# Performance work log

Hardware: AMD Instinct MI355X
Metric: run time of the kernel (lower is better)

## Reference

```python
import jax, jax.numpy as jnp
import numpy as np

FEAT_DIM = 128
GUIDE_DIM = 128
HIDDEN = [1024, 512, 256, 128]
OUT_DIM = 2


def make_coord(shape):
    # grid-center coords in (-1, 1), matching the torch make_coord
    seqs = [(-1.0 + 1.0 / n) + (2.0 / n) * jnp.arange(n, dtype=jnp.float32) for n in shape]
    yy, xx = jnp.meshgrid(seqs[0], seqs[1], indexing='ij')
    return jnp.stack([yy, xx], axis=-1)  # [h, w, 2]


def grid_sample_nearest(img, coord):
    # img: [B, C, H, W]; coord: [B, N, 2] with coord[...,0] along H, coord[...,1] along W
    # replicates F.grid_sample(img, coord.flip(-1)..., mode='nearest', align_corners=False,
    # padding_mode='zeros') followed by permute -> [B, N, C]
    B, C, H, W = img.shape
    iy = jnp.round(((coord[..., 0] + 1.0) * H - 1.0) * 0.5)
    ix = jnp.round(((coord[..., 1] + 1.0) * W - 1.0) * 0.5)
    valid = (iy >= 0) & (iy < H) & (ix >= 0) & (ix < W)
    iyc = jnp.clip(iy, 0, H - 1).astype(jnp.int32)
    ixc = jnp.clip(ix, 0, W - 1).astype(jnp.int32)
    g = jax.vmap(lambda im, y, x: im[:, y, x])(img, iyc, ixc)  # [B, C, N]
    g = g * valid[:, None, :].astype(img.dtype)  # zero padding outside
    return jnp.transpose(g, (0, 2, 1))  # [B, N, C]


def mlp(x, params):
    for W, b in params[:-1]:
        x = jax.nn.relu(x @ W + b)
    W, b = params[-1]
    return x @ W + b


def setup_inputs() -> dict:
    key = jax.random.key(0)
    ks = jax.random.split(key, 16)
    B, h, w = 4, 64, 64
    H_hr = W_hr = 256
    N = H_hr * W_hr  # 65536 query points
    feat = jax.random.normal(ks[0], (B, FEAT_DIM, h, w), jnp.float32)
    coord = jax.random.uniform(ks[1], (B, N, 2), jnp.float32, minval=-1.0, maxval=1.0)
    hr_guide = jax.random.normal(ks[2], (B, GUIDE_DIM, H_hr, W_hr), jnp.float32)
    lr_guide = jax.random.normal(ks[3], (B, GUIDE_DIM, h, w), jnp.float32)
    in_dim = FEAT_DIM + 2 * GUIDE_DIM + 2  # 386
    dims = [in_dim] + HIDDEN + [OUT_DIM]
    inp = {"feat": feat, "coord": coord, "hr_guide": hr_guide, "lr_guide": lr_guide}
    for i in range(len(dims) - 1):
        scale = 1.0 / np.sqrt(dims[i]).astype(np.float32)
        inp[f"W{i}"] = jax.random.normal(ks[4 + 2 * i], (dims[i], dims[i + 1]), jnp.float32) * scale
        inp[f"b{i}"] = jnp.zeros((dims[i + 1],), jnp.float32)
    return inp


def reference(feat, coord, hr_guide, lr_guide, W0, b0, W1, b1, W2, b2, W3, b3, W4, b4):
    params = [(W0, b0), (W1, b1), (W2, b2), (W3, b3), (W4, b4)]
    B, C, h, w = feat.shape
    N = coord.shape[1]
    fc = make_coord((h, w))  # [h, w, 2]
    feat_coord = jnp.broadcast_to(jnp.transpose(fc, (2, 0, 1))[None], (B, 2, h, w))
    q_guide_hr = grid_sample_nearest(hr_guide, coord)  # [B, N, G]
    rx = 1.0 / h
    ry = 1.0 / w
    hw = jnp.array([h, w], dtype=coord.dtype)
    preds = []
    for vx in (-1.0, 1.0):
        for vy in (-1.0, 1.0):
            shift = jnp.array([vx * rx, vy * ry], dtype=coord.dtype)
            coord_ = coord + shift
            q_feat = grid_sample_nearest(feat, coord_)        # [B, N, C]
            q_coord = grid_sample_nearest(feat_coord, coord_)  # [B, N, 2]
            rel_coord = (coord - q_coord) * hw                 # [B, N, 2]
            q_guide_lr = grid_sample_nearest(lr_guide, coord_)  # [B, N, G]
            inp = jnp.concatenate([q_feat, q_guide_hr, q_guide_hr - q_guide_lr, rel_coord], axis=-1)
            pred = mlp(inp.reshape(B * N, -1), params).reshape(B, N, OUT_DIM)
            preds.append(pred)
    preds = jnp.stack(preds, axis=-1)  # [B, N, 2, 4]
    weight = jax.nn.softmax(preds[:, :, 1, :], axis=-1)  # [B, N, 4]
    ret = jnp.sum(preds[:, :, 0, :] * weight, axis=-1, keepdims=True)  # [B, N, 1]
    return ret
```

## Files before the change

kernel.cpp:

```cpp
#include <hip/hip_runtime.h>
#include <cstdint>
#include <cstddef>


typedef unsigned short u16;
typedef unsigned int u32;
typedef _Float16 half8 __attribute__((ext_vector_type(8)));
typedef float floatx4 __attribute__((ext_vector_type(4)));
typedef float floatx2 __attribute__((ext_vector_type(2)));
typedef u32 u32x2 __attribute__((ext_vector_type(2)));
typedef u32 u32x4 __attribute__((ext_vector_type(4)));

__device__ __forceinline__ u16 f2h(float x) {
    _Float16 h = (_Float16)x;
    return __builtin_bit_cast(unsigned short, h);
}
__device__ __forceinline__ float h2f(u16 u) {
    return (float)__builtin_bit_cast(_Float16, u);
}

__device__ __forceinline__ void cp_async16(const void* gsrc, void* lds) {
#if defined(__has_builtin) && __has_builtin(__builtin_amdgcn_global_load_lds)
    __builtin_amdgcn_global_load_lds(
        (__attribute__((address_space(1))) void*)(uintptr_t)gsrc,
        (__attribute__((address_space(3))) void*)(uint32_t)(uintptr_t)lds,
        16, 0, 0);
#else
    *(u32x4*)lds = *(const u32x4*)gsrc;
#endif
}

__global__ void transpose_chw_hwc(const float* __restrict__ src,
                                  u16* __restrict__ dst, int HW) {
    __shared__ float t[32][33];
    const int b = blockIdx.z;
    const int hw0 = blockIdx.x * 32, c0 = blockIdx.y * 32;
    const float* s = src + (size_t)b * 128 * HW;
    u16* d = dst + (size_t)b * HW * 128;
    const int tx = threadIdx.x, ty = threadIdx.y;
#pragma unroll
    for (int j = 0; j < 4; ++j)
        t[ty + j * 8][tx] = s[(size_t)(c0 + ty + j * 8) * HW + hw0 + tx];
    __syncthreads();
#pragma unroll
    for (int j = 0; j < 4; ++j)
        d[(size_t)(hw0 + ty + j * 8) * 128 + c0 + tx] = f2h(t[tx][ty + j * 8]);
}

__global__ void prep_wt(const float* __restrict__ W, u16* __restrict__ Wt,
                        int K, int N, int perm) {
    int idx = blockIdx.x * 256 + threadIdx.x;
    if (idx >= N * K) return;
    int nn = idx / K, kk = idx - nn * K;
    int ka = kk;
    if (perm) {
        int s = kk & 63;
        ka = (kk & ~63) + ((s & 3) << 4) + (s >> 2);
    }
    Wt[idx] = f2h(W[(size_t)ka * N + nn]);
}

__global__ void prep_w0(const float* __restrict__ W0, u16* __restrict__ Wt0m,
                        u16* __restrict__ Wthr) {
    int idx = blockIdx.x * 256 + threadIdx.x;
    if (idx < 1024 * 256) {
        int n = idx >> 8, k = idx & 255;
        float v = (k < 128) ? W0[(size_t)k * 1024 + n]
                            : -W0[(size_t)(128 + k) * 1024 + n];
        Wt0m[idx] = f2h(v);
    }
    if (idx < 1024 * 128) {
        int n = idx >> 7, k = idx & 127;
        Wthr[idx] = f2h(W0[(size_t)(128 + k) * 1024 + n] +
                        W0[(size_t)(256 + k) * 1024 + n]);
    }
}

__global__ __launch_bounds__(256) void gather_build(
    const float* __restrict__ coord, const u16* __restrict__ hrT,
    const u16* __restrict__ featT, const u16* __restrict__ lrT,
    u16* __restrict__ X, u16* __restrict__ Qhr, float* __restrict__ rel,
    int p0) {
    const int wid = threadIdx.x >> 6, lane = threadIdx.x & 63;
    const int pl = blockIdx.x * 4 + wid;
    const int p = p0 + pl;
    const int b = p >> 16;
    const float cy = coord[(size_t)p * 2];
    const float cx = coord[(size_t)p * 2 + 1];
    const u32* hr32 = (const u32*)hrT;
    const u32* ft32 = (const u32*)featT;
    const u32* lr32 = (const u32*)lrT;

    float fy = rintf(((cy + 1.0f) * 256.0f - 1.0f) * 0.5f);
    float fx = rintf(((cx + 1.0f) * 256.0f - 1.0f) * 0.5f);
    bool vh = (fy >= 0.0f) && (fy < 256.0f) && (fx >= 0.0f) && (fx < 256.0f);
    int iy = (int)fminf(fmaxf(fy, 0.0f), 255.0f);
    int ix = (int)fminf(fmaxf(fx, 0.0f), 255.0f);
    u32 hrv = hr32[((((size_t)b * 256 + iy) * 256 + ix) * 128 >> 1) + lane];
    if (!vh) hrv = 0u;
    ((u32*)Qhr)[(size_t)pl * 64 + lane] = hrv;

    const size_t rowbase = (size_t)pl * 4;
#pragma unroll
    for (int s = 0; s < 4; ++s) {
        float sy = (s & 2) ? 0.015625f : -0.015625f;
        float sx = (s & 1) ? 0.015625f : -0.015625f;
        float gy = rintf(((cy + sy + 1.0f) * 64.0f - 1.0f) * 0.5f);
        float gx = rintf(((cx + sx + 1.0f) * 64.0f - 1.0f) * 0.5f);
        bool v = (gy >= 0.0f) && (gy < 64.0f) && (gx >= 0.0f) && (gx < 64.0f);
        int jy = (int)fminf(fmaxf(gy, 0.0f), 63.0f);
        int jx = (int)fminf(fmaxf(gx, 0.0f), 63.0f);
        size_t g32 = ((((size_t)b * 64 + jy) * 64 + jx) * 128 >> 1) + lane;
        u32 fv = ft32[g32];
        u32 lv = lr32[g32];
        if (!v) { fv = 0u; lv = 0u; }

        u32* xr = (u32*)(X + (rowbase + s) * 256);
        xr[lane] = fv;
        xr[64 + lane] = lv;

        if (lane == 0) {
            float qcy = v ? (-0.984375f + 0.03125f * (float)jy) : 0.0f;
            float qcx = v ? (-0.984375f + 0.03125f * (float)jx) : 0.0f;
            rel[(rowbase + s) * 2 + 0] = (cy - qcy) * 64.0f;
            rel[(rowbase + s) * 2 + 1] = (cx - qcx) * 64.0f;
        }
    }
}

__global__ __launch_bounds__(512, 2) void gemm_f16_256(
    const u16* __restrict__ A, const u16* __restrict__ Bt,
    const float* __restrict__ bias, u16* __restrict__ C, int K, int N,
    int lognb, const float* __restrict__ rel, const float* __restrict__ w0tail) {
    __shared__ __align__(16) u16 sA[2][2][8192];
    __shared__ __align__(16) u16 sB[2][2][8192];
    const int tid = threadIdx.x;
    const int lane = tid & 63;
    const int wid = tid >> 6;
    const int r = lane & 15, q = lane >> 4;
    const int wm = wid >> 2, wn = wid & 3;

    const int g = blockIdx.x;
    const int n_idx = (g >> 3) & ((1 << lognb) - 1);
    const int m_idx = (g & 7) + ((g >> (3 + lognb)) << 3);
    const int n0 = n_idx << 8;
    const u32 m0 = (u32)m_idx << 8;

    const u32 srow = (u32)(tid >> 2);
    const u32 gchunk = (u32)((tid & 3) ^ ((tid >> 3) & 3));
    const u32 gaoff = (m0 + srow) * (u32)K + (gchunk << 3);
    const u32 gboff = ((u32)n0 + srow) * (u32)K + (gchunk << 3);

    auto stageA = [&](int kt, int ks, int buf) {
        const u16* gp = A + gaoff + (u32)((kt << 6) + (ks << 5));
        u16* lp = &sA[buf][ks][tid << 3];
        cp_async16(gp, lp);
        cp_async16(gp + ((u32)K << 7), lp + 4096);
    };
    auto stageB = [&](int kt, int ks, int buf) {
        const u16* gp = Bt + gboff + (u32)((kt << 6) + (ks << 5));
        u16* lp = &sB[buf][ks][tid << 3];
        cp_async16(gp, lp);
        cp_async16(gp + ((u32)K << 7), lp + 4096);
    };

    const int fs = (q ^ ((r >> 1) & 3)) << 3;
    const int abase = ((wm << 7) + r) * 32 + fs;
    const int bbase = ((wn << 6) + r) * 32 + fs;

    floatx4 acc[8][4];
#pragma unroll
    for (int mi = 0; mi < 8; ++mi)
#pragma unroll
        for (int ni = 0; ni < 4; ++ni)
            acc[mi][ni] = (floatx4){0.0f, 0.0f, 0.0f, 0.0f};

    const int nk = K >> 6;
    stageA(0, 0, 0);
    stageA(0, 1, 0);
    stageB(0, 0, 0);
    stageB(0, 1, 0);
    const int k1 = (nk > 1) ? 1 : 0;
    stageA(k1, 0, 1);
    stageA(k1, 1, 1);
    stageB(k1, 1, 1);
    asm volatile("s_waitcnt vmcnt(6)");
    __builtin_amdgcn_s_barrier();

    half8 a0[8], a1[8], bf[2], bg[2];
    for (int kt = 0; kt < nk; ++kt) {
        const int cur = kt & 1, nxt = cur ^ 1;
        const bool p1 = (kt + 1) < nk;
        const bool p2 = (kt + 2) < nk;
#pragma unroll
        for (int mi = 0; mi < 8; ++mi)
            a0[mi] = *(const half8*)&sA[cur][0][abase + (mi << 9)];
#pragma unroll
        for (int ni = 0; ni < 2; ++ni)
            bf[ni] = *(const half8*)&sB[cur][0][bbase + (ni << 9)];
        if (p1) stageB(kt + 1, 0, nxt);
#pragma unroll
        for (int mi = 0; mi < 8; ++mi)
            a1[mi] = *(const half8*)&sA[cur][1][abase + (mi << 9)];
#pragma unroll
        for (int ni = 0; ni < 2; ++ni)
            bg[ni] = *(const half8*)&sB[cur][1][bbase + (ni << 9)];
        __builtin_amdgcn_s_setprio(1);
#pragma unroll
        for (int mi = 0; mi < 8; ++mi)
#pragma unroll
            for (int ni = 0; ni < 2; ++ni)
                acc[mi][ni] = __builtin_amdgcn_mfma_f32_16x16x32_f16(
                    a0[mi], bf[ni], acc[mi][ni], 0, 0, 0);
        __builtin_amdgcn_s_setprio(0);
        __builtin_amdgcn_s_barrier();
        if (p2) stageA(kt + 2, 0, cur);
#pragma unroll
        for (int ni = 0; ni < 2; ++ni)
            bf[ni] = *(const half8*)&sB[cur][1][bbase + 1024 + (ni << 9)];
        __builtin_amdgcn_s_setprio(1);
#pragma unroll
        for (int mi = 0; mi < 8; ++mi)
#pragma unroll
            for (int ni = 0; ni < 2; ++ni)
                acc[mi][ni] = __builtin_amdgcn_mfma_f32_16x16x32_f16(
                    a1[mi], bg[ni], acc[mi][ni], 0, 0, 0);
        __builtin_amdgcn_s_setprio(0);
        __builtin_amdgcn_s_barrier();
        if (p2) stageA(kt + 2, 1, cur);
#pragma unroll
        for (int ni = 0; ni < 2; ++ni)
            bg[ni] = *(const half8*)&sB[cur][0][bbase + 1024 + (ni << 9)];
        __builtin_amdgcn_s_setprio(1);
#pragma unroll
        for (int mi = 0; mi < 8; ++mi)
#pragma unroll
            for (int ni = 0; ni < 2; ++ni)
                acc[mi][2 + ni] = __builtin_amdgcn_mfma_f32_16x16x32_f16(
                    a1[mi], bf[ni], acc[mi][2 + ni], 0, 0, 0);
        __builtin_amdgcn_s_setprio(0);
        __builtin_amdgcn_s_barrier();
        if (p2) stageB(kt + 2, 1, cur);
        __builtin_amdgcn_s_setprio(1);
#pragma unroll
        for (int mi = 0; mi < 8; ++mi)
#pragma unroll
            for (int ni = 0; ni < 2; ++ni)
                acc[mi][2 + ni] = __builtin_amdgcn_mfma_f32_16x16x32_f16(
                    a0[mi], bg[ni], acc[mi][2 + ni], 0, 0, 0);
        __builtin_amdgcn_s_setprio(0);
        if (p2) {
            asm volatile("s_waitcnt vmcnt(6)");
        } else {
            asm volatile("s_waitcnt vmcnt(0)");
        }
        __builtin_amdgcn_s_barrier();
    }

    float bias_v[4], w0a[4], w0b[4];
#pragma unroll
    for (int nig = 0; nig < 4; ++nig) {
        int col = n0 + (wn << 6) + nig * 16 + r;
        bias_v[nig] = bias[col];
        w0a[nig] = rel ? w0tail[col] : 0.0f;
        w0b[nig] = rel ? w0tail[N + col] : 0.0f;
    }
#pragma unroll
    for (int mi = 0; mi < 8; ++mi) {
#pragma unroll
        for (int rr = 0; rr < 4; ++rr) {
            u32 row = m0 + (u32)(wm << 7) + (u32)(mi << 4) + (u32)(q << 2) +
                      (u32)rr;
            float rl0 = 0.0f, rl1 = 0.0f;
            if (rel) {
                floatx2 rl = *(const floatx2*)&rel[(size_t)row * 2];
                rl0 = rl[0];
                rl1 = rl[1];
            }
            u32 pk[2];
#pragma unroll
            for (int h = 0; h < 2; ++h) {
                u32 w = 0;
#pragma unroll
                for (int j = 0; j < 2; ++j) {
                    int nig = h * 2 + j;
                    float v = acc[mi][nig][rr] + bias_v[nig];
                    if (rel) v += rl0 * w0a[nig] + rl1 * w0b[nig];
                    v = fmaxf(v, 0.0f);
                    w |= (u32)f2h(v) << (16 * j);
                }
                pk[h] = w;
            }
            *(u32x2*)(C + row * (u32)N + (u32)(n0 + (wn << 6) + (r << 2))) =
                (u32x2){pk[0], pk[1]};
        }
    }
}

__global__ __launch_bounds__(256, 3) void gemm_f16(
    const u16* __restrict__ A, const u16* __restrict__ Bt,
    const float* __restrict__ bias, u16* __restrict__ C, int K, int N,
    int lognb, const float* __restrict__ rel, const float* __restrict__ w0tail,
    const u16* __restrict__ hq, int doRelu) {
    __shared__ __align__(16) u16 As[2][128 * 64];
    __shared__ __align__(16) u16 Bs[128 * 64];
    const int tid = threadIdx.x;
    const int lane = tid & 63;
    const int wid = tid >> 6;
    const int r = lane & 15, q = lane >> 4;
    const int wm = (wid & 1) << 6, wn = (wid >> 1) << 6;

    const int g = blockIdx.x;
    const int n_idx = (g >> 3) & ((1 << lognb) - 1);
    const int m_idx = (g & 7) + ((g >> (3 + lognb)) << 3);
    const int n0 = n_idx << 7;
    const u32 m0 = (u32)m_idx << 7;

    const int srow = tid >> 3;
    const int schunk = (tid & 7) ^ (srow & 7);
    const u32 gaoff = (m0 + (u32)srow) * (u32)K + ((u32)schunk << 3);
    const u32 gboff = (u32)(n0 + srow) * (u32)K + ((u32)schunk << 3);

    auto stageA = [&](int kt, int buf) {
        const u16* gak = A + gaoff + (kt << 6);
        u16* la = &As[buf][tid * 8];
#pragma unroll
        for (int i = 0; i < 4; ++i)
            cp_async16(gak + (u32)(i << 5) * (u32)K, la + (i << 11));
    };

    u32x4 breg[4];
    auto loadB = [&](int kt) {
        const u16* gbk = Bt + gboff + (kt << 6);
#pragma unroll
        for (int i = 0; i < 4; ++i)
            breg[i] = *(const u32x4*)(gbk + (u32)(i << 5) * (u32)K);
    };
    auto writeB = [&]() {
        u16* lb = &Bs[tid * 8];
#pragma unroll
        for (int i = 0; i < 4; ++i)
            *(u32x4*)(lb + (i << 11)) = breg[i];
    };

    const int cx = (q ^ (r & 7)) << 3;
    const int arow = (wm + r) << 6, brow = (wn + r) << 6;

    floatx4 acc[4][4];
#pragma unroll
    for (int mi = 0; mi < 4; ++mi)
#pragma unroll
        for (int ni = 0; ni < 4; ++ni)
            acc[mi][ni] = (floatx4){0.0f, 0.0f, 0.0f, 0.0f};

    const int nk = K >> 6;
    loadB(0);
    stageA(0, 0);
    writeB();
    __syncthreads();

    for (int kt = 0; kt < nk; ++kt) {
        const int cur = kt & 1;
        const bool pf = (kt + 1 < nk);
        if (pf) {
            loadB(kt + 1);
            stageA(kt + 1, cur ^ 1);
        }
#pragma unroll
        for (int ks = 0; ks < 2; ++ks) {
            half8 af[4], bfr[4];
#pragma unroll
            for (int mi = 0; mi < 4; ++mi)
                af[mi] = *(const half8*)&As[cur][arow + (mi << 10) + (cx ^ (ks << 5))];
#pragma unroll
            for (int ni = 0; ni < 4; ++ni)
                bfr[ni] = *(const half8*)&Bs[brow + (ni << 10) + (cx ^ (ks << 5))];
#pragma unroll
            for (int mi = 0; mi < 4; ++mi)
#pragma unroll
                for (int ni = 0; ni < 4; ++ni)
                    acc[mi][ni] = __builtin_amdgcn_mfma_f32_16x16x32_f16(
                        af[mi], bfr[ni], acc[mi][ni], 0, 0, 0);
        }
        if (pf) {
            __syncthreads();
            writeB();
            __syncthreads();
        }
    }

    float bias_v[4], w0a[4], w0b[4];
#pragma unroll
    for (int ni = 0; ni < 4; ++ni) {
        int col = n0 + wn + ni * 16 + r;
        bias_v[ni] = bias ? bias[col] : 0.0f;
        w0a[ni] = rel ? w0tail[col] : 0.0f;
        w0b[ni] = rel ? w0tail[N + col] : 0.0f;
    }
#pragma unroll
    for (int mi = 0; mi < 4; ++mi) {
        float addv[4];
        if (hq) {
            u32 pidx = ((m0 + (u32)wm + (u32)(mi << 4)) >> 2) + (u32)q;
            u32x2 hv = *(const u32x2*)(hq + (size_t)pidx * (u32)N +
                                       (u32)(n0 + wn + (r << 2)));
            addv[0] = h2f((u16)(hv[0] & 0xffffu));
            addv[1] = h2f((u16)(hv[0] >> 16));
            addv[2] = h2f((u16)(hv[1] & 0xffffu));
            addv[3] = h2f((u16)(hv[1] >> 16));
        } else {
#pragma unroll
            for (int ni = 0; ni < 4; ++ni) addv[ni] = bias_v[ni];
        }
#pragma unroll
        for (int rr = 0; rr < 4; ++rr) {
            u32 row = m0 + wm + mi * 16 + q * 4 + rr;
            float rl0 = 0.0f, rl1 = 0.0f;
            if (rel) {
                floatx2 rl = *(const floatx2*)&rel[(size_t)row * 2];
                rl0 = rl[0];
                rl1 = rl[1];
            }
            u32 pk[2];
#pragma unroll
            for (int h = 0; h < 2; ++h) {
                u32 w = 0;
#pragma unroll
                for (int j = 0; j < 2; ++j) {
                    int ni = h * 2 + j;
                    float v = acc[mi][ni][rr] + addv[ni];
                    if (rel) v += rl0 * w0a[ni] + rl1 * w0b[ni];
                    if (doRelu) v = fmaxf(v, 0.0f);
                    w |= (u32)f2h(v) << (16 * j);
                }
                pk[h] = w;
            }
            *(u32x2*)(C + row * (u32)N + (u32)(n0 + wn + (r << 2))) =
                (u32x2){pk[0], pk[1]};
        }
    }
}

__global__ __launch_bounds__(256, 3) void gemm_l3l4(
    const u16* __restrict__ A, const u16* __restrict__ Bt,
    const float* __restrict__ b3, const float* __restrict__ W4,
    const float* __restrict__ b4, float* __restrict__ out, int p0) {
    __shared__ __align__(16) u16 As[2][128 * 64];
    __shared__ __align__(16) u16 Bs[128 * 64];
    __shared__ float sums[2][2][64][2];
    const int K = 256;
    const int tid = threadIdx.x;
    const int lane = tid & 63;
    const int wid = tid >> 6;
    const int r = lane & 15, q = lane >> 4;
    const int wm1 = wid & 1, wn1 = wid >> 1;
    const int wm = wm1 << 6, wn = wn1 << 6;
    const u32 m0 = (u32)blockIdx.x << 7;

    const int srow = tid >> 3;
    const int schunk = (tid & 7) ^ (srow & 7);
    const u32 gaoff = (m0 + (u32)srow) * (u32)K + ((u32)schunk << 3);
    const u32 gboff = (u32)srow * (u32)K + ((u32)schunk << 3);

    auto stageA = [&](int kt, int buf) {
        const u16* gak = A + gaoff + (kt << 6);
        u16* la = &As[buf][tid * 8];
#pragma unroll
        for (int i = 0; i < 4; ++i)
            cp_async16(gak + (u32)(i << 5) * (u32)K, la + (i << 11));
    };

    u32x4 breg[4];
    auto loadB = [&](int kt) {
        const u16* gbk = Bt + gboff + (kt << 6);
#pragma unroll
        for (int i = 0; i < 4; ++i)
            breg[i] = *(const u32x4*)(gbk + (u32)(i << 5) * (u32)K);
    };
    auto writeB = [&]() {
        u16* lb = &Bs[tid * 8];
#pragma unroll
        for (int i = 0; i < 4; ++i)
            *(u32x4*)(lb + (i << 11)) = breg[i];
    };

    const int cx = (q ^ (r & 7)) << 3;
    const int arow = (wm + r) << 6, brow = (wn + r) << 6;

    floatx4 acc[4][4];
#pragma unroll
    for (int mi = 0; mi < 4; ++mi)
#pragma unroll
        for (int ni = 0; ni < 4; ++ni)
            acc[mi][ni] = (floatx4){0.0f, 0.0f, 0.0f, 0.0f};

    const int nk = K >> 6;
    loadB(0);
    stageA(0, 0);
    writeB();
    __syncthreads();
    for (int kt = 0; kt < nk; ++kt) {
        const int cur = kt & 1;
        const bool pf = (kt + 1 < nk);
        if (pf) {
            loadB(kt + 1);
            stageA(kt + 1, cur ^ 1);
        }
#pragma unroll
        for (int ks = 0; ks < 2; ++ks) {
            half8 af[4], bfr[4];
#pragma unroll
            for (int mi = 0; mi < 4; ++mi)
                af[mi] = *(const half8*)&As[cur][arow + (mi << 10) + (cx ^ (ks << 5))];
#pragma unroll
            for (int ni = 0; ni < 4; ++ni)
                bfr[ni] = *(const half8*)&Bs[brow + (ni << 10) + (cx ^ (ks << 5))];
#pragma unroll
            for (int mi = 0; mi < 4; ++mi)
#pragma unroll
                for (int ni = 0; ni < 4; ++ni)
                    acc[mi][ni] = __builtin_amdgcn_mfma_f32_16x16x32_f16(
                        af[mi], bfr[ni], acc[mi][ni], 0, 0, 0);
        }
        if (pf) {
            __syncthreads();
            writeB();
            __syncthreads();
        }
    }

    float b3v[4], w40[4], w41[4];
#pragma unroll
    for (int ni = 0; ni < 4; ++ni) {
        int ch = wn + ni * 16 + r;
        b3v[ni] = b3[ch];
        w40[ni] = W4[ch * 2];
        w41[ni] = W4[ch * 2 + 1];
    }
#pragma unroll
    for (int mi = 0; mi < 4; ++mi) {
#pragma unroll
        for (int rr = 0; rr < 4; ++rr) {
            float d0 = 0.0f, d1 = 0.0f;
#pragma unroll
            for (int ni = 0; ni < 4; ++ni) {
                float v = fmaxf(acc[mi][ni][rr] + b3v[ni], 0.0f);
                d0 += v * w40[ni];
                d1 += v * w41[ni];
            }
#pragma unroll
            for (int m = 1; m <= 8; m <<= 1) {
                d0 += __shfl_xor(d0, m, 64);
                d1 += __shfl_xor(d1, m, 64);
            }
            if (r == 0) {
                int rl = mi * 16 + q * 4 + rr;
                sums[wm1][wn1][rl][0] = d0;
                sums[wm1][wn1][rl][1] = d1;
            }
        }
    }
    __syncthreads();
    if (tid < 32) {
        const int pl = tid;
        const int w = pl >> 4;
        const int rb = (pl & 15) * 4;
        float P0[4], P1[4];
#pragma unroll
        for (int s = 0; s < 4; ++s) {
            P0[s] = sums[w][0][rb + s][0] + sums[w][1][rb + s][0] + b4[0];
            P1[s] = sums[w][0][rb + s][1] + sums[w][1][rb + s][1] + b4[1];
        }
        float mx = fmaxf(fmaxf(P1[0], P1[1]), fmaxf(P1[2], P1[3]));
        float e0 = __expf(P1[0] - mx), e1 = __expf(P1[1] - mx);
        float e2 = __expf(P1[2] - mx), e3 = __expf(P1[3] - mx);
        float se = e0 + e1 + e2 + e3;
        out[p0 + (int)(m0 >> 2) + pl] =
            (P0[0] * e0 + P0[1] * e1 + P0[2] * e2 + P0[3] * e3) / se;
    }
}

extern "C" void kernel_launch(void* const* d_in, const int* in_sizes, int n_in,
                              void* d_out, int out_size, void* d_ws,
                              size_t ws_size, hipStream_t stream) {
    const float* feat = (const float*)d_in[0];
    const float* coord = (const float*)d_in[1];
    const float* hr = (const float*)d_in[2];
    const float* lr = (const float*)d_in[3];
    const float* W0 = (const float*)d_in[4];
    const float* b0 = (const float*)d_in[5];
    const float* W1 = (const float*)d_in[6];
    const float* b1 = (const float*)d_in[7];
    const float* W2 = (const float*)d_in[8];
    const float* b2 = (const float*)d_in[9];
    const float* W3 = (const float*)d_in[10];
    const float* b3 = (const float*)d_in[11];
    const float* W4 = (const float*)d_in[12];
    const float* b4 = (const float*)d_in[13];
    float* out = (float*)d_out;

    char* base = (char*)d_ws;
    size_t off = 0;
    auto carve = [&](size_t bytes) -> char* {
        char* p = base + off;
        off += (bytes + 255) & ~(size_t)255;
        return p;
    };

    u16* hrT = (u16*)carve(4ull * 65536 * 128 * 2);
    u16* featT = (u16*)carve(4ull * 4096 * 128 * 2);
    u16* lrT = (u16*)carve(4ull * 4096 * 128 * 2);
    u16* Wt0m = (u16*)carve(1024ull * 256 * 2);
    u16* Wthr = (u16*)carve(1024ull * 128 * 2);
    u16* Wt1 = (u16*)carve(512ull * 1024 * 2);
    u16* Wt2 = (u16*)carve(256ull * 512 * 2);
    u16* Wt3 = (u16*)carve(128ull * 256 * 2);
    const size_t fixed = off;

    const size_t R = 1048576ull;
    int c = 16;
    for (; c < 8192; c *= 2) {
        size_t Rc = R / c;
        size_t need = fixed;
        size_t sizes[3] = {Rc * 1024, Rc * 8, Rc * 2048};
        for (int i = 0; i < 3; ++i) need += (sizes[i] + 255) & ~(size_t)255;
        if (need <= ws_size) break;
    }
    const size_t Rc = R / c;
    const int Pc = (int)(262144 / c);

    char* R1 = carve(Rc * 1024);
    float* rel = (float*)carve(Rc * 8);
    char* R2 = carve(Rc * 2048);
    u16* X = (u16*)R1;
    u16* H = (u16*)(R1 + Rc * 512);
    u16* A1 = (u16*)R1;
    u16* Qhr = (u16*)R2;
    u16* A0 = (u16*)R2;
    u16* A2 = (u16*)R2;

    transpose_chw_hwc<<<dim3(2048, 4, 4), dim3(32, 8), 0, stream>>>(hr, hrT, 65536);
    transpose_chw_hwc<<<dim3(128, 4, 4), dim3(32, 8), 0, stream>>>(feat, featT, 4096);
    transpose_chw_hwc<<<dim3(128, 4, 4), dim3(32, 8), 0, stream>>>(lr, lrT, 4096);
    prep_w0<<<1024, 256, 0, stream>>>(W0, Wt0m, Wthr);
    prep_wt<<<(512 * 1024 + 255) / 256, 256, 0, stream>>>(W1, Wt1, 1024, 512, 1);
    prep_wt<<<(256 * 512 + 255) / 256, 256, 0, stream>>>(W2, Wt2, 512, 256, 1);
    prep_wt<<<(128 * 256 + 255) / 256, 256, 0, stream>>>(W3, Wt3, 256, 128, 1);

    const int mt1 = (int)(Rc / 128);
    const int mt2 = (int)(Rc / 256);
    const int mth = (int)(Rc / 512);
    const bool use256 = (Rc % 2048ull) == 0;
    for (int ci = 0; ci < c; ++ci) {
        const int p0 = ci * Pc;
        gather_build<<<Pc / 4, 256, 0, stream>>>(coord, hrT, featT, lrT, X, Qhr,
                                                 rel, p0);
        gemm_f16<<<mth * 8, 256, 0, stream>>>(Qhr, Wthr, b0, H, 128, 1024, 3,
                                              nullptr, nullptr, nullptr, 0);
        gemm_f16<<<mt1 * 8, 256, 0, stream>>>(X, Wt0m, nullptr, A0, 256, 1024,
                                              3, rel, W0 + 384 * 1024, H, 1);
        if (use256) {
            gemm_f16_256<<<mt2 * 2, 512, 0, stream>>>(A0, Wt1, b1, A1, 1024, 512,
                                                      1, nullptr, nullptr);
            gemm_f16_256<<<mt2 * 1, 512, 0, stream>>>(A1, Wt2, b2, A2, 512, 256,
                                                      0, nullptr, nullptr);
        } else {
            gemm_f16<<<mt1 * 4, 256, 0, stream>>>(A0, Wt1, b1, A1, 1024, 512, 2,
                                                  nullptr, nullptr, nullptr, 1);
            gemm_f16<<<mt1 * 2, 256, 0, stream>>>(A1, Wt2, b2, A2, 512, 256, 1,
                                                  nullptr, nullptr, nullptr, 1);
        }
        gemm_l3l4<<<mt1, 256, 0, stream>>>(A2, Wt3, b3, W4, b4, out, p0);
    }
}
```

Before: 3.454 ms.

## Prefetch next k-tile fragments into registers during last MFMA phase

Reorders the four MFMA phases of the GEMM main loop and moves the LDS reads of the next k-tile's first A/B fragments into the current iteration, ahead of the final MFMA block. The vmcnt wait and barrier move earlier so the next buffer is ready. The goal is to hide LDS read latency at the top of each iteration behind MFMA work. In exchange the barrier and waitcnt placement gets more intricate and must stay correct for the double-buffered staging, with some risk of extra register pressure.

```diff
diff --git a/kernel.cpp b/kernel.cpp
--- a/kernel.cpp
+++ b/kernel.cpp
@@ -187,75 +187,85 @@
     asm volatile("s_waitcnt vmcnt(6)");
     __builtin_amdgcn_s_barrier();
 
-    half8 a0[8], a1[8], bf[2], bg[2];
+    half8 a0[8], a1[8], bA[2], bB[2];
+#pragma unroll
+    for (int mi = 0; mi < 8; ++mi)
+        a0[mi] = *(const half8*)&sA[0][0][abase + (mi << 9)];
+#pragma unroll
+    for (int ni = 0; ni < 2; ++ni)
+        bA[ni] = *(const half8*)&sB[0][0][bbase + (ni << 9)];
+
     for (int kt = 0; kt < nk; ++kt) {
         const int cur = kt & 1, nxt = cur ^ 1;
         const bool p1 = (kt + 1) < nk;
         const bool p2 = (kt + 2) < nk;
-#pragma unroll
-        for (int mi = 0; mi < 8; ++mi)
-            a0[mi] = *(const half8*)&sA[cur][0][abase + (mi << 9)];
-#pragma unroll
-        for (int ni = 0; ni < 2; ++ni)
-            bf[ni] = *(const half8*)&sB[cur][0][bbase + (ni << 9)];
         if (p1) stageB(kt + 1, 0, nxt);
 #pragma unroll
         for (int mi = 0; mi < 8; ++mi)
             a1[mi] = *(const half8*)&sA[cur][1][abase + (mi << 9)];
 #pragma unroll
         for (int ni = 0; ni < 2; ++ni)
-            bg[ni] = *(const half8*)&sB[cur][1][bbase + (ni << 9)];
+            bB[ni] = *(const half8*)&sB[cur][0][bbase + 1024 + (ni << 9)];
         __builtin_amdgcn_s_setprio(1);
 #pragma unroll
         for (int mi = 0; mi < 8; ++mi)
 #pragma unroll
             for (int ni = 0; ni < 2; ++ni)
                 acc[mi][ni] = __builtin_amdgcn_mfma_f32_16x16x32_f16(
-                    a0[mi], bf[ni], acc[mi][ni], 0, 0, 0);
+                    a0[mi], bA[ni], acc[mi][ni], 0, 0, 0);
         __builtin_amdgcn_s_setprio(0);
         __builtin_amdgcn_s_barrier();
         if (p2) stageA(kt + 2, 0, cur);
 #pragma unroll
         for (int ni = 0; ni < 2; ++ni)
-            bf[ni] = *(const half8*)&sB[cur][1][bbase + 1024 + (ni << 9)];
+            bA[ni] = *(const half8*)&sB[cur][1][bbase + (ni << 9)];
         __builtin_amdgcn_s_setprio(1);
 #pragma unroll
         for (int mi = 0; mi < 8; ++mi)
 #pragma unroll
             for (int ni = 0; ni < 2; ++ni)
-                acc[mi][ni] = __builtin_amdgcn_mfma_f32_16x16x32_f16(
-                    a1[mi], bg[ni], acc[mi][ni], 0, 0, 0);
+                acc[mi][2 + ni] = __builtin_amdgcn_mfma_f32_16x16x32_f16(
+                    a0[mi], bB[ni], acc[mi][2 + ni], 0, 0, 0);
         __builtin_amdgcn_s_setprio(0);
         __builtin_amdgcn_s_barrier();
         if (p2) stageA(kt + 2, 1, cur);
 #pragma unroll
         for (int ni = 0; ni < 2; ++ni)
-            bg[ni] = *(const half8*)&sB[cur][0][bbase + 1024 + (ni << 9)];
+            bB[ni] = *(const half8*)&sB[cur][1][bbase + 1024 + (ni << 9)];
+        __builtin_amdgcn_s_setprio(1);
+#pragma unroll
+        for (int mi = 0; mi < 8; ++mi)
+#pragma unroll
+            for (int ni = 0; ni < 2; ++ni)
+                acc[mi][ni] = __builtin_amdgcn_mfma_f32_16x16x32_f16(
+                    a1[mi], bA[ni], acc[mi][ni], 0, 0, 0);
+        __builtin_amdgcn_s_setprio(0);
+        if (p2) {
+            asm volatile("s_waitcnt vmcnt(4)");
+        } else if (p1) {
+            asm volatile("s_waitcnt vmcnt(0)");
+        }
+        __builtin_amdgcn_s_barrier();
+        if (p2) stageB(kt + 2, 1, cur);
+        if (p1) {
+#pragma unroll
+            for (int mi = 0; mi < 8; ++mi)
+                a0[mi] = *(const half8*)&sA[nxt][0][abase + (mi << 9)];
+#pragma unroll
+            for (int ni = 0; ni < 2; ++ni)
+                bA[ni] = *(const half8*)&sB[nxt][0][bbase + (ni << 9)];
+        }
         __builtin_amdgcn_s_setprio(1);
 #pragma unroll
         for (int mi = 0; mi < 8; ++mi)
 #pragma unroll
             for (int ni = 0; ni < 2; ++ni)
                 acc[mi][2 + ni] = __builtin_amdgcn_mfma_f32_16x16x32_f16(
-                    a1[mi], bf[ni], acc[mi][2 + ni], 0, 0, 0);
+                    a1[mi], bB[ni], acc[mi][2 + ni], 0, 0, 0);
         __builtin_amdgcn_s_setprio(0);
         __builtin_amdgcn_s_barrier();
-        if (p2) stageB(kt + 2, 1, cur);
-        __builtin_amdgcn_s_setprio(1);
-#pragma unroll
-        for (int mi = 0; mi < 8; ++mi)
-#pragma unroll
-            for (int ni = 0; ni < 2; ++ni)
-                acc[mi][2 + ni] = __builtin_amdgcn_mfma_f32_16x16x32_f16(
-                    a0[mi], bg[ni], acc[mi][2 + ni], 0, 0, 0);
-        __builtin_amdgcn_s_setprio(0);
-        if (p2) {
-            asm volatile("s_waitcnt vmcnt(6)");
-        } else {
-            asm volatile("s_waitcnt vmcnt(0)");
-        }
-        __builtin_amdgcn_s_barrier();
-    }
+    }
+    asm volatile("s_waitcnt vmcnt(0)");
 
     float bias_v[4], w0a[4], w0b[4];
 #pragma unroll
```

New measurement: 3.637 ms. +5.3%, slower.
